# Optimization experiments

Hardware: AMD Instinct MI355X
Metric: run time of the kernel (lower is better)

Reference implementation:

```python
import jax, jax.numpy as jnp
import numpy as np

LAMBDA = 10.0      # sinkhorn_lambda from init_kwargs
N_ITERS = 100      # fixed Sinkhorn iteration count
B, T_MAX, D_MAX = 256, 256, 256
TP, DP = T_MAX + 1, D_MAX + 1   # expanded with births/deaths row+col
L = TP * DP                      # padded flat output length per example
EPS = 1e-12


def setup_inputs() -> dict:
    key = jax.random.key(0)
    k1, k2, k3 = jax.random.split(key, 3)
    affinity_scores = jax.random.uniform(k1, (B, T_MAX, D_MAX), dtype=jnp.float32)
    num_detections = jax.random.randint(k2, (B,), 32, D_MAX + 1, dtype=jnp.int32)
    num_tracklets = jax.random.randint(k3, (B,), 32, T_MAX + 1, dtype=jnp.int32)
    return {
        "affinity_scores": affinity_scores,
        "num_detections": num_detections,
        "num_tracklets": num_tracklets,
    }


def _sinkhorn_transport(aff, nd, nt):
    """Masked Sinkhorn on the expanded (nt+1)x(nd+1) matrix, padded to [TP,DP]."""
    r = jnp.arange(TP)
    c = jnp.arange(DP)
    row_valid = r <= nt          # nt tracklet rows + 1 births/deaths row
    col_valid = c <= nd
    interior = (r[:, None] < nt) & (c[None, :] < nd)
    aff_pad = jnp.pad(aff, ((0, 1), (0, 1)))
    aff_e = jnp.where(interior, aff_pad, 0.0)   # dummy row/col have affinity 0
    mask = (row_valid[:, None] & col_valid[None, :]).astype(aff.dtype)
    # cost = -affinity  =>  kernel K = exp(-lambda * cost) = exp(lambda * affinity)
    K = jnp.exp(LAMBDA * aff_e) * mask
    ndf = nd.astype(aff.dtype)
    ntf = nt.astype(aff.dtype)
    # target marginals: [1,...,1, length] on valid entries, 0 on padding
    row_sums = jnp.where(r < nt, 1.0, jnp.where(r == nt, ndf, 0.0))
    col_sums = jnp.where(c < nd, 1.0, jnp.where(c == nd, ntf, 0.0))
    u0 = jnp.zeros((TP,), aff.dtype)
    v0 = col_valid.astype(aff.dtype)

    def body(carry, _):
        u, v = carry
        u = jnp.where(row_valid, row_sums / (K @ v + EPS), 0.0)
        v = jnp.where(col_valid, col_sums / (K.T @ u + EPS), 0.0)
        return (u, v), None

    (u, v), _ = jax.lax.scan(body, (u0, v0), None, length=N_ITERS)
    transport = u[:, None] * K * v[None, :]
    return transport, interior, row_valid, col_valid


def _single(aff, nd, nt):
    transport, interior, row_valid, col_valid = _sinkhorn_transport(aff, nd, nt)
    r = jnp.arange(TP)
    c = jnp.arange(DP)

    # hard assignment on transport[:-1,:-1] (valid interior): mutual argmax
    neg_inf = jnp.array(-jnp.inf, transport.dtype)
    t_in = jnp.where(interior, transport, neg_inf)
    row_max = jnp.max(t_in, axis=1, keepdims=True)
    col_max = jnp.max(t_in, axis=0, keepdims=True)
    assign_in = interior & (t_in == row_max) & (t_in == col_max)
    # births/deaths: unmatched tracklets -> death col nd; unmatched detections -> birth row nt
    row_has = jnp.any(assign_in, axis=1)
    col_has = jnp.any(assign_in, axis=0)
    deaths = (r[:, None] < nt) & (c[None, :] == nd) & (~row_has)[:, None]
    births = (r[:, None] == nt) & (c[None, :] < nd) & (~col_has)[None, :]
    assignment = assign_in | deaths | births

    # flatten the (nt+1)x(nd+1) valid submatrix row-major, zero-pad to length L
    k = jnp.arange(L)
    length = (nt + 1) * (nd + 1)
    rr = jnp.clip(k // (nd + 1), 0, T_MAX)
    cc = k % (nd + 1)
    valid = k < length
    t_flat = jnp.where(valid, transport[rr, cc], 0.0)
    a_flat = jnp.where(valid, assignment[rr, cc], False)
    return t_flat, a_flat


def reference(affinity_scores, num_detections, num_tracklets):
    t_flat, a_flat = jax.vmap(_single)(affinity_scores, num_detections, num_tracklets)
    return t_flat, a_flat
```

## Files before the change

### kernel.cpp

```cpp
#include <hip/hip_runtime.h>


#define T_MAX   256
#define L_FLAT  (257 * 257)
#define N_ITERS 100
#define LAMBDA_F 10.0f
#define EPS_F    1e-12f

#define ROR1 0x121
#define ROR2 0x122
#define ROR4 0x124
#define ROR8 0x128

typedef short bf8   __attribute__((ext_vector_type(8)));
typedef float f32x4 __attribute__((ext_vector_type(4)));

struct F4 { float a, b, c, d; };

template<int CTRL>
__device__ __forceinline__ float dpp_addf(float x) {
    int t = __builtin_amdgcn_update_dpp(0, __float_as_int(x), CTRL, 0xF, 0xF, true);
    return x + __int_as_float(t);
}
__device__ __forceinline__ float swz16_addf(float x) {
    return x + __int_as_float(__builtin_amdgcn_ds_swizzle(__float_as_int(x), 0x401F));
}
__device__ __forceinline__ float swz16_maxf(float x) {
    return fmaxf(x, __int_as_float(__builtin_amdgcn_ds_swizzle(__float_as_int(x), 0x401F)));
}
__device__ __forceinline__ int swz16_ori(int x) {
    return x | __builtin_amdgcn_ds_swizzle(x, 0x401F);
}
__device__ __forceinline__ float fast_rcp(float x) {
#if __has_builtin(__builtin_amdgcn_rcpf)
    return __builtin_amdgcn_rcpf(x);
#else
    return 1.0f / x;
#endif
}
__device__ __forceinline__ unsigned short f2bf(float x) {
    unsigned u = __float_as_uint(x);
    return (unsigned short)((u + 0x7FFFu + ((u >> 16) & 1u)) >> 16);
}
__device__ __forceinline__ float bf2f(short s) {
    return __uint_as_float(((unsigned)(unsigned short)s) << 16);
}

__global__ __launch_bounds__(1024, 1) void assoc_sinkhorn_kernel(
    const float* __restrict__ aff,
    const int*   __restrict__ ndet,
    const int*   __restrict__ ntrk,
    float*       __restrict__ out_t,
    float*       __restrict__ out_a)
{
    const int b   = blockIdx.x;
    const int nd  = ndet[b];
    const int nt  = ntrk[b];
    const int tid = threadIdx.x;
    const int w   = tid >> 6;
    const int l   = tid & 63;
    const int lr  = l & 15;
    const int lk  = l >> 4;

    __shared__ __align__(16) unsigned short KTL[16 * 8 * 64 * 8];
    __shared__ __align__(16) unsigned short u_bf[256];
    __shared__ __align__(16) unsigned short v_bf[256];
    __shared__ __align__(16) float u_f[256];
    __shared__ __align__(16) float v_f[256];
    __shared__ __align__(16) float SuAcc[2];
    __shared__ __align__(16) float SvAcc[2];
    __shared__ __align__(16) float rm_s[256];
    __shared__ __align__(16) float cm_s[256];

    const float ndf = (float)nd;
    const float ntf = (float)nt;

    bf8 KA[8];
    const float* Ab = aff + (size_t)b * (T_MAX * T_MAX);

    const int myrow = 16 * w + lr;
    const int mycol = 16 * w + lr;
    unsigned short* myKTL = &KTL[(size_t)(w * 8 * 64 + l) * 8];

    {
        const bool rv = (myrow < nt);
        const float* rp = Ab + (size_t)myrow * T_MAX;
        #pragma unroll
        for (int t = 0; t < 8; ++t) {
            const int c0 = 32 * t + 8 * lk;
            const float4 x0 = *reinterpret_cast<const float4*>(rp + c0);
            const float4 x1 = *reinterpret_cast<const float4*>(rp + c0 + 4);
            const float e[8] = {x0.x, x0.y, x0.z, x0.w, x1.x, x1.y, x1.z, x1.w};
            bf8 kk;
            #pragma unroll
            for (int j = 0; j < 8; ++j) {
                const float val = (rv && (c0 + j) < nd) ? __expf(LAMBDA_F * e[j]) : 0.0f;
                kk[j] = (short)f2bf(val);
            }
            KA[t] = kk;
        }
    }
    {
        const bool cv = (mycol < nd);
        #pragma unroll
        for (int t = 0; t < 8; ++t) {
            const int r0 = 32 * t + 8 * lk;
            bf8 kk;
            #pragma unroll
            for (int j = 0; j < 8; ++j) {
                const float x = Ab[(size_t)(r0 + j) * T_MAX + mycol];
                const float val = (cv && (r0 + j) < nt) ? __expf(LAMBDA_F * x) : 0.0f;
                kk[j] = (short)f2bf(val);
            }
            *reinterpret_cast<bf8*>(myKTL + t * 512) = kk;
        }
    }

    if (tid < 256) v_bf[tid] = (tid < nd) ? f2bf(1.0f) : (unsigned short)0;
    if (tid == 0) {
        SuAcc[0] = 0.0f; SuAcc[1] = 0.0f;
        SvAcc[0] = ndf;  SvAcc[1] = 0.0f;
    }
    __syncthreads();

    float vbd = 1.0f;
    float ubd = 0.0f;

    const int r_a0 = 16 * w + 4 * lk;
    float u4[4] = {0.f, 0.f, 0.f, 0.f};
    float v0 = 0.0f;

    float rvm[4];
    #pragma unroll
    for (int q = 0; q < 4; ++q) rvm[q] = ((r_a0 + q) < nt) ? 1.0f : 0.0f;
    const float cvm = (mycol < nd) ? 1.0f : 0.0f;

    for (int it = 0; it < N_ITERS; ++it) {
        const int p = it & 1;
        const float Sv = SvAcc[p];

        f32x4 acc = {0.0f, 0.0f, 0.0f, 0.0f};
        #pragma unroll
        for (int t = 0; t < 8; ++t) {
            const bf8 VF = *reinterpret_cast<const bf8*>(&v_bf[32 * t + 8 * lk]);
            acc = __builtin_amdgcn_mfma_f32_16x16x32_bf16(KA[t], VF, acc, 0, 0, 0);
        }

        const float vbdE = vbd + EPS_F;
        #pragma unroll
        for (int q = 0; q < 4; ++q)
            u4[q] = rvm[q] * fast_rcp(acc[q] + vbdE);

        {
            float su = (u4[0] + u4[1]) + (u4[2] + u4[3]);
            su = swz16_addf(su);
            su += __shfl_xor(su, 32, 64);
            if (l == 0) atomicAdd(&SuAcc[p], su);
        }
        if (tid == 0) SuAcc[p ^ 1] = 0.0f;

        if (lr == 0) {
            const unsigned p01 = (unsigned)f2bf(u4[0]) | ((unsigned)f2bf(u4[1]) << 16);
            const unsigned p23 = (unsigned)f2bf(u4[2]) | ((unsigned)f2bf(u4[3]) << 16);
            *reinterpret_cast<uint2*>(&u_bf[r_a0]) = uint2{p01, p23};
        }
        __syncthreads();

        const float Su = SuAcc[p];
        const float ubd_new = ndf * fast_rcp(Sv + vbd + EPS_F);
        const float vbd_new = ntf * fast_rcp(Su + ubd_new + EPS_F);

        f32x4 qa = {0.0f, 0.0f, 0.0f, 0.0f};
        #pragma unroll
        for (int t = 0; t < 8; ++t) {
            const bf8 UF = *reinterpret_cast<const bf8*>(&u_bf[32 * t + 8 * lk]);
            const bf8 kb = *reinterpret_cast<const bf8*>(myKTL + t * 512);
            qa = __builtin_amdgcn_mfma_f32_16x16x32_bf16(UF, kb, qa, 0, 0, 0);
        }

        const float ubdE = ubd_new + EPS_F;
        v0 = cvm * fast_rcp(qa[0] + ubdE);

        {
            float sv = v0;
            sv = dpp_addf<ROR1>(sv);
            sv = dpp_addf<ROR2>(sv);
            sv = dpp_addf<ROR4>(sv);
            sv = dpp_addf<ROR8>(sv);
            if (l == 0) atomicAdd(&SvAcc[p ^ 1], sv);
        }
        if (tid == 0) SvAcc[p] = 0.0f;
        if (lk == 0) v_bf[mycol] = f2bf(v0);
        ubd = ubd_new;
        vbd = vbd_new;
        __syncthreads();
    }

    if (lr == 0) {
        f32x4 uf = {u4[0], u4[1], u4[2], u4[3]};
        *reinterpret_cast<f32x4*>(&u_f[r_a0]) = uf;
    }
    if (lk == 0) v_f[mycol] = v0;
    __syncthreads();

    float rm;
    {
        const float ur = u_f[myrow];
        float mm = 0.0f;
        #pragma unroll
        for (int t = 0; t < 8; ++t) {
            const f32x4 va = *reinterpret_cast<const f32x4*>(&v_f[32 * t + 8 * lk]);
            const f32x4 vb = *reinterpret_cast<const f32x4*>(&v_f[32 * t + 8 * lk + 4]);
            const float vj[8] = {va[0], va[1], va[2], va[3], vb[0], vb[1], vb[2], vb[3]};
            #pragma unroll
            for (int j = 0; j < 8; ++j) {
                const float tv = ur * bf2f(KA[t][j]) * vj[j];
                mm = fmaxf(mm, tv);
            }
        }
        mm = swz16_maxf(mm);
        mm = fmaxf(mm, __shfl_xor(mm, 32, 64));
        rm = mm;
        if (lk == 0) rm_s[myrow] = mm;
    }
    float cmv;
    {
        const float vc = v_f[mycol];
        float mm = 0.0f;
        #pragma unroll
        for (int t = 0; t < 8; ++t) {
            const int rb = 32 * t + 8 * lk;
            const bf8 kb = *reinterpret_cast<const bf8*>(myKTL + t * 512);
            const f32x4 ua = *reinterpret_cast<const f32x4*>(&u_f[rb]);
            const f32x4 ub = *reinterpret_cast<const f32x4*>(&u_f[rb + 4]);
            const float uj[8] = {ua[0], ua[1], ua[2], ua[3], ub[0], ub[1], ub[2], ub[3]};
            #pragma unroll
            for (int j = 0; j < 8; ++j) {
                const float tv = uj[j] * bf2f(kb[j]) * vc;
                mm = fmaxf(mm, tv);
            }
        }
        mm = swz16_maxf(mm);
        mm = fmaxf(mm, __shfl_xor(mm, 32, 64));
        cmv = mm;
        if (lk == 0) cm_s[mycol] = mm;
    }
    __syncthreads();

    float* Ot = out_t + (size_t)b * L_FLAT;
    float* Oa = out_a + (size_t)b * L_FLAT;
    const int stride = nd + 1;

    {
        const float vc = v_f[mycol];
        const bool cv = (mycol < nd);
        int has = 0;
        #pragma unroll
        for (int t = 0; t < 8; ++t) {
            const int rb = 32 * t + 8 * lk;
            const bf8 kb = *reinterpret_cast<const bf8*>(myKTL + t * 512);
            const f32x4 ua = *reinterpret_cast<const f32x4*>(&u_f[rb]);
            const f32x4 ub = *reinterpret_cast<const f32x4*>(&u_f[rb + 4]);
            const f32x4 ra = *reinterpret_cast<const f32x4*>(&rm_s[rb]);
            const f32x4 rb4 = *reinterpret_cast<const f32x4*>(&rm_s[rb + 4]);
            const float uj[8] = {ua[0], ua[1], ua[2], ua[3], ub[0], ub[1], ub[2], ub[3]};
            const float rj[8] = {ra[0], ra[1], ra[2], ra[3], rb4[0], rb4[1], rb4[2], rb4[3]};
            #pragma unroll
            for (int j = 0; j < 8; ++j) {
                const int rowj = rb + j;
                const float tv = uj[j] * bf2f(kb[j]) * vc;
                const bool bit = (rowj < nt) && cv && (tv == rj[j]) && (tv == cmv);
                has |= bit ? 1 : 0;
            }
        }
        has = swz16_ori(has);
        has |= __shfl_xor(has, 32, 64);
        if (lk == 0 && cv) {
            const int kk = nt * stride + mycol;
            Ot[kk] = ubd * vc;
            Oa[kk] = has ? 0.0f : 1.0f;
        }
    }
    if (tid == 0) {
        const int kk = nt * stride + nd;
        Ot[kk] = ubd * vbd;
        Oa[kk] = 0.0f;
    }

    {
        const float ur = u_f[myrow];
        const bool rv = (myrow < nt);
        int has = 0;
        #pragma unroll
        for (int t = 0; t < 8; ++t) {
            const int cb = 32 * t + 8 * lk;
            const f32x4 va  = *reinterpret_cast<const f32x4*>(&v_f[cb]);
            const f32x4 vb  = *reinterpret_cast<const f32x4*>(&v_f[cb + 4]);
            const f32x4 ca  = *reinterpret_cast<const f32x4*>(&cm_s[cb]);
            const f32x4 cb4 = *reinterpret_cast<const f32x4*>(&cm_s[cb + 4]);
            float tvs[8];
            float abs_[8];
            #pragma unroll
            for (int j = 0; j < 4; ++j) {
                const float tv = ur * bf2f(KA[t][j]) * va[j];
                const bool bit = rv && ((cb + j) < nd) && (tv == rm) && (tv == ca[j]);
                tvs[j] = tv; abs_[j] = bit ? 1.0f : 0.0f;
                has |= bit ? 1 : 0;
            }
            #pragma unroll
            for (int j = 0; j < 4; ++j) {
                const float tv = ur * bf2f(KA[t][4 + j]) * vb[j];
                const bool bit = rv && ((cb + 4 + j) < nd) && (tv == rm) && (tv == cb4[j]);
                tvs[4 + j] = tv; abs_[4 + j] = bit ? 1.0f : 0.0f;
                has |= bit ? 1 : 0;
            }
            if (rv) {
                float* OtR = Ot + (size_t)myrow * stride;
                float* OaR = Oa + (size_t)myrow * stride;
                #pragma unroll
                for (int g = 0; g < 2; ++g) {
                    const int c0 = cb + 4 * g;
                    if (c0 + 3 < nd) {
                        F4 ot = {tvs[4*g], tvs[4*g+1], tvs[4*g+2], tvs[4*g+3]};
                        F4 oa = {abs_[4*g], abs_[4*g+1], abs_[4*g+2], abs_[4*g+3]};
                        *reinterpret_cast<F4*>(OtR + c0) = ot;
                        *reinterpret_cast<F4*>(OaR + c0) = oa;
                    } else {
                        #pragma unroll
                        for (int j = 0; j < 4; ++j) {
                            if (c0 + j < nd) {
                                OtR[c0 + j] = tvs[4*g + j];
                                OaR[c0 + j] = abs_[4*g + j];
                            }
                        }
                    }
                }
            }
        }
        has = swz16_ori(has);
        has |= __shfl_xor(has, 32, 64);
        if (lk == 0 && rv) {
            const int kk = myrow * stride + nd;
            Ot[kk] = ur * vbd;
            Oa[kk] = has ? 0.0f : 1.0f;
        }
    }

    const int length = (nt + 1) * stride;
    for (int k = length + tid; k < L_FLAT; k += 1024) {
        Ot[k] = 0.0f;
        Oa[k] = 0.0f;
    }
}

extern "C" void kernel_launch(void* const* d_in, const int* in_sizes, int n_in,
                              void* d_out, int out_size, void* d_ws, size_t ws_size,
                              hipStream_t stream)
{
    const float* aff  = (const float*)d_in[0];
    const int*   ndet = (const int*)d_in[1];
    const int*   ntrk = (const int*)d_in[2];
    const int    Bn   = in_sizes[1];
    float* out_t = (float*)d_out;
    float* out_a = out_t + (size_t)Bn * L_FLAT;
    assoc_sinkhorn_kernel<<<dim3(Bn), dim3(1024), 0, stream>>>(aff, ndet, ntrk, out_t, out_a);
}
```

Baseline: 392.2 us.

## Replace MFMA K^T·u matvec with packed-bf16 scalar FMA dot products

The second Sinkhorn half-step (K^T u) no longer uses 16x16x32 MFMA, where only one output column of the 16 was useful. It now computes each column dot product with scalar FMAs over packed bf16 pairs. Each lane handles two columns over a 32-row slice, and the partial sums are reduced with DPP quad permutes and swizzles. The transposed K storage in shared memory is re-laid out as packed u32 pairs to match, and the post-loop column max and assignment checks are rewritten for the new layout. This removes the wasted MFMA work, but adds more VALU instructions and cross-lane reduction steps to every iteration.

```diff
diff --git a/kernel.cpp b/kernel.cpp
--- a/kernel.cpp
+++ b/kernel.cpp
@@ -7,13 +7,15 @@
 #define LAMBDA_F 10.0f
 #define EPS_F    1e-12f
 
-#define ROR1 0x121
-#define ROR2 0x122
-#define ROR4 0x124
-#define ROR8 0x128
+#define QX1   0xB1
+#define QX2   0x4E
+#define SWZ4  0x101F
+#define SWZ8  0x201F
+#define SWZ16 0x401F
 
 typedef short bf8   __attribute__((ext_vector_type(8)));
 typedef float f32x4 __attribute__((ext_vector_type(4)));
+typedef unsigned int u32x4 __attribute__((ext_vector_type(4)));
 
 struct F4 { float a, b, c, d; };
 
@@ -22,14 +24,27 @@
     int t = __builtin_amdgcn_update_dpp(0, __float_as_int(x), CTRL, 0xF, 0xF, true);
     return x + __int_as_float(t);
 }
-__device__ __forceinline__ float swz16_addf(float x) {
-    return x + __int_as_float(__builtin_amdgcn_ds_swizzle(__float_as_int(x), 0x401F));
-}
-__device__ __forceinline__ float swz16_maxf(float x) {
-    return fmaxf(x, __int_as_float(__builtin_amdgcn_ds_swizzle(__float_as_int(x), 0x401F)));
-}
-__device__ __forceinline__ int swz16_ori(int x) {
-    return x | __builtin_amdgcn_ds_swizzle(x, 0x401F);
+template<int CTRL>
+__device__ __forceinline__ float dpp_maxf(float x) {
+    int t = __builtin_amdgcn_update_dpp(0, __float_as_int(x), CTRL, 0xF, 0xF, true);
+    return fmaxf(x, __int_as_float(t));
+}
+template<int CTRL>
+__device__ __forceinline__ int dpp_ori(int x) {
+    int t = __builtin_amdgcn_update_dpp(0, x, CTRL, 0xF, 0xF, true);
+    return x | t;
+}
+template<int OFF>
+__device__ __forceinline__ float swz_addf(float x) {
+    return x + __int_as_float(__builtin_amdgcn_ds_swizzle(__float_as_int(x), OFF));
+}
+template<int OFF>
+__device__ __forceinline__ float swz_maxf(float x) {
+    return fmaxf(x, __int_as_float(__builtin_amdgcn_ds_swizzle(__float_as_int(x), OFF)));
+}
+template<int OFF>
+__device__ __forceinline__ int swz_ori(int x) {
+    return x | __builtin_amdgcn_ds_swizzle(x, OFF);
 }
 __device__ __forceinline__ float fast_rcp(float x) {
 #if __has_builtin(__builtin_amdgcn_rcpf)
@@ -44,6 +59,12 @@
 }
 __device__ __forceinline__ float bf2f(short s) {
     return __uint_as_float(((unsigned)(unsigned short)s) << 16);
+}
+__device__ __forceinline__ float bflo(unsigned u) {
+    return __uint_as_float(u << 16);
+}
+__device__ __forceinline__ float bfhi(unsigned u) {
+    return __uint_as_float(u & 0xFFFF0000u);
 }
 
 __global__ __launch_bounds__(1024, 1) void assoc_sinkhorn_kernel(
@@ -61,8 +82,10 @@
     const int l   = tid & 63;
     const int lr  = l & 15;
     const int lk  = l >> 4;
-
-    __shared__ __align__(16) unsigned short KTL[16 * 8 * 64 * 8];
+    const int cp  = l >> 3;
+    const int rc  = l & 7;
+
+    __shared__ __align__(16) unsigned KCL[16 * 8 * 64 * 4];
     __shared__ __align__(16) unsigned short u_bf[256];
     __shared__ __align__(16) unsigned short v_bf[256];
     __shared__ __align__(16) float u_f[256];
@@ -79,40 +102,48 @@
     const float* Ab = aff + (size_t)b * (T_MAX * T_MAX);
 
     const int myrow = 16 * w + lr;
-    const int mycol = 16 * w + lr;
-    unsigned short* myKTL = &KTL[(size_t)(w * 8 * 64 + l) * 8];
+    const int c0    = 16 * w + 2 * cp;
+    unsigned* myKC0 = &KCL[((w * 8 + 0) * 64 + l) * 4];
+    unsigned* myKC1 = &KCL[((w * 8 + 4) * 64 + l) * 4];
 
     {
         const bool rv = (myrow < nt);
         const float* rp = Ab + (size_t)myrow * T_MAX;
         #pragma unroll
         for (int t = 0; t < 8; ++t) {
-            const int c0 = 32 * t + 8 * lk;
-            const float4 x0 = *reinterpret_cast<const float4*>(rp + c0);
-            const float4 x1 = *reinterpret_cast<const float4*>(rp + c0 + 4);
+            const int cc0 = 32 * t + 8 * lk;
+            const float4 x0 = *reinterpret_cast<const float4*>(rp + cc0);
+            const float4 x1 = *reinterpret_cast<const float4*>(rp + cc0 + 4);
             const float e[8] = {x0.x, x0.y, x0.z, x0.w, x1.x, x1.y, x1.z, x1.w};
             bf8 kk;
             #pragma unroll
             for (int j = 0; j < 8; ++j) {
-                const float val = (rv && (c0 + j) < nd) ? __expf(LAMBDA_F * e[j]) : 0.0f;
+                const float val = (rv && (cc0 + j) < nd) ? __expf(LAMBDA_F * e[j]) : 0.0f;
                 kk[j] = (short)f2bf(val);
             }
             KA[t] = kk;
         }
     }
     {
-        const bool cv = (mycol < nd);
-        #pragma unroll
-        for (int t = 0; t < 8; ++t) {
-            const int r0 = 32 * t + 8 * lk;
-            bf8 kk;
-            #pragma unroll
-            for (int j = 0; j < 8; ++j) {
-                const float x = Ab[(size_t)(r0 + j) * T_MAX + mycol];
-                const float val = (cv && (r0 + j) < nt) ? __expf(LAMBDA_F * x) : 0.0f;
-                kk[j] = (short)f2bf(val);
-            }
-            *reinterpret_cast<bf8*>(myKTL + t * 512) = kk;
+        #pragma unroll
+        for (int j = 0; j < 2; ++j) {
+            const int col = c0 + j;
+            const bool cv = (col < nd);
+            unsigned* dst = (j == 0) ? myKC0 : myKC1;
+            #pragma unroll
+            for (int g = 0; g < 4; ++g) {
+                u32x4 pk;
+                #pragma unroll
+                for (int s = 0; s < 4; ++s) {
+                    const int r = 32 * rc + 8 * g + 2 * s;
+                    const float x0 = Ab[(size_t)r * T_MAX + col];
+                    const float x1 = Ab[(size_t)(r + 1) * T_MAX + col];
+                    const float f0 = (cv && r     < nt) ? __expf(LAMBDA_F * x0) : 0.0f;
+                    const float f1 = (cv && r + 1 < nt) ? __expf(LAMBDA_F * x1) : 0.0f;
+                    pk[s] = (unsigned)f2bf(f0) | ((unsigned)f2bf(f1) << 16);
+                }
+                *reinterpret_cast<u32x4*>(dst + g * 256) = pk;
+            }
         }
     }
 
@@ -128,12 +159,13 @@
 
     const int r_a0 = 16 * w + 4 * lk;
     float u4[4] = {0.f, 0.f, 0.f, 0.f};
-    float v0 = 0.0f;
+    float v0 = 0.0f, v1 = 0.0f;
 
     float rvm[4];
     #pragma unroll
     for (int q = 0; q < 4; ++q) rvm[q] = ((r_a0 + q) < nt) ? 1.0f : 0.0f;
-    const float cvm = (mycol < nd) ? 1.0f : 0.0f;
+    const float cvm0 = (c0     < nd) ? 1.0f : 0.0f;
+    const float cvm1 = (c0 + 1 < nd) ? 1.0f : 0.0f;
 
     for (int it = 0; it < N_ITERS; ++it) {
         const int p = it & 1;
@@ -153,7 +185,7 @@
 
         {
             float su = (u4[0] + u4[1]) + (u4[2] + u4[3]);
-            su = swz16_addf(su);
+            su = swz_addf<SWZ16>(su);
             su += __shfl_xor(su, 32, 64);
             if (l == 0) atomicAdd(&SuAcc[p], su);
         }
@@ -170,27 +202,43 @@
         const float ubd_new = ndf * fast_rcp(Sv + vbd + EPS_F);
         const float vbd_new = ntf * fast_rcp(Su + ubd_new + EPS_F);
 
-        f32x4 qa = {0.0f, 0.0f, 0.0f, 0.0f};
-        #pragma unroll
-        for (int t = 0; t < 8; ++t) {
-            const bf8 UF = *reinterpret_cast<const bf8*>(&u_bf[32 * t + 8 * lk]);
-            const bf8 kb = *reinterpret_cast<const bf8*>(myKTL + t * 512);
-            qa = __builtin_amdgcn_mfma_f32_16x16x32_bf16(UF, kb, qa, 0, 0, 0);
-        }
-
         const float ubdE = ubd_new + EPS_F;
-        v0 = cvm * fast_rcp(qa[0] + ubdE);
-
+        float t0 = 0.0f, t1 = 0.0f;
         {
-            float sv = v0;
-            sv = dpp_addf<ROR1>(sv);
-            sv = dpp_addf<ROR2>(sv);
-            sv = dpp_addf<ROR4>(sv);
-            sv = dpp_addf<ROR8>(sv);
+            const u32x4* ub = reinterpret_cast<const u32x4*>(&u_bf[32 * rc]);
+            #pragma unroll
+            for (int g = 0; g < 4; ++g) {
+                const u32x4 U  = ub[g];
+                const u32x4 K0 = *reinterpret_cast<const u32x4*>(myKC0 + g * 256);
+                const u32x4 K1 = *reinterpret_cast<const u32x4*>(myKC1 + g * 256);
+                #pragma unroll
+                for (int s = 0; s < 4; ++s) {
+                    const float ulo = bflo(U[s]);
+                    const float uhi = bfhi(U[s]);
+                    t0 = fmaf(bflo(K0[s]), ulo, t0);
+                    t0 = fmaf(bfhi(K0[s]), uhi, t0);
+                    t1 = fmaf(bflo(K1[s]), ulo, t1);
+                    t1 = fmaf(bfhi(K1[s]), uhi, t1);
+                }
+            }
+        }
+        t0 = dpp_addf<QX1>(t0); t0 = dpp_addf<QX2>(t0); t0 = swz_addf<SWZ4>(t0);
+        t1 = dpp_addf<QX1>(t1); t1 = dpp_addf<QX2>(t1); t1 = swz_addf<SWZ4>(t1);
+
+        v0 = cvm0 * fast_rcp(t0 + ubdE);
+        v1 = cvm1 * fast_rcp(t1 + ubdE);
+
+        {
+            float sv = v0 + v1;
+            sv = swz_addf<SWZ8>(sv);
+            sv = swz_addf<SWZ16>(sv);
+            sv += __shfl_xor(sv, 32, 64);
             if (l == 0) atomicAdd(&SvAcc[p ^ 1], sv);
         }
         if (tid == 0) SvAcc[p] = 0.0f;
-        if (lk == 0) v_bf[mycol] = f2bf(v0);
+        if (rc == 0)
+            *reinterpret_cast<unsigned*>(&v_bf[c0]) =
+                (unsigned)f2bf(v0) | ((unsigned)f2bf(v1) << 16);
         ubd = ubd_new;
         vbd = vbd_new;
         __syncthreads();
@@ -200,7 +248,10 @@
         f32x4 uf = {u4[0], u4[1], u4[2], u4[3]};
         *reinterpret_cast<f32x4*>(&u_f[r_a0]) = uf;
     }
-    if (lk == 0) v_f[mycol] = v0;
+    if (rc == 0) {
+        v_f[c0]     = v0;
+        v_f[c0 + 1] = v1;
+    }
     __syncthreads();
 
     float rm;
@@ -218,32 +269,36 @@
                 mm = fmaxf(mm, tv);
             }
         }
-        mm = swz16_maxf(mm);
+        mm = swz_maxf<SWZ16>(mm);
         mm = fmaxf(mm, __shfl_xor(mm, 32, 64));
         rm = mm;
         if (lk == 0) rm_s[myrow] = mm;
     }
-    float cmv;
-    {
-        const float vc = v_f[mycol];
-        float mm = 0.0f;
-        #pragma unroll
-        for (int t = 0; t < 8; ++t) {
-            const int rb = 32 * t + 8 * lk;
-            const bf8 kb = *reinterpret_cast<const bf8*>(myKTL + t * 512);
-            const f32x4 ua = *reinterpret_cast<const f32x4*>(&u_f[rb]);
-            const f32x4 ub = *reinterpret_cast<const f32x4*>(&u_f[rb + 4]);
-            const float uj[8] = {ua[0], ua[1], ua[2], ua[3], ub[0], ub[1], ub[2], ub[3]};
-            #pragma unroll
-            for (int j = 0; j < 8; ++j) {
-                const float tv = uj[j] * bf2f(kb[j]) * vc;
-                mm = fmaxf(mm, tv);
-            }
-        }
-        mm = swz16_maxf(mm);
-        mm = fmaxf(mm, __shfl_xor(mm, 32, 64));
-        cmv = mm;
-        if (lk == 0) cm_s[mycol] = mm;
+    float cmv0 = 0.0f, cmv1 = 0.0f;
+    {
+        const float vc0 = v_f[c0];
+        const float vc1 = v_f[c0 + 1];
+        #pragma unroll
+        for (int g = 0; g < 4; ++g) {
+            const u32x4 K0 = *reinterpret_cast<const u32x4*>(myKC0 + g * 256);
+            const u32x4 K1 = *reinterpret_cast<const u32x4*>(myKC1 + g * 256);
+            const f32x4 ua  = *reinterpret_cast<const f32x4*>(&u_f[32 * rc + 8 * g]);
+            const f32x4 ub2 = *reinterpret_cast<const f32x4*>(&u_f[32 * rc + 8 * g + 4]);
+            const float uu[8] = {ua[0], ua[1], ua[2], ua[3], ub2[0], ub2[1], ub2[2], ub2[3]};
+            #pragma unroll
+            for (int s = 0; s < 4; ++s) {
+                cmv0 = fmaxf(cmv0, fmaxf((uu[2*s] * bflo(K0[s])) * vc0,
+                                         (uu[2*s+1] * bfhi(K0[s])) * vc0));
+                cmv1 = fmaxf(cmv1, fmaxf((uu[2*s] * bflo(K1[s])) * vc1,
+                                         (uu[2*s+1] * bfhi(K1[s])) * vc1));
+            }
+        }
+        cmv0 = dpp_maxf<QX1>(cmv0); cmv0 = dpp_maxf<QX2>(cmv0); cmv0 = swz_maxf<SWZ4>(cmv0);
+        cmv1 = dpp_maxf<QX1>(cmv1); cmv1 = dpp_maxf<QX2>(cmv1); cmv1 = swz_maxf<SWZ4>(cmv1);
+        if (rc == 0) {
+            cm_s[c0]     = cmv0;
+            cm_s[c0 + 1] = cmv1;
+        }
     }
     __syncthreads();
 
@@ -252,33 +307,45 @@
     const int stride = nd + 1;
 
     {
-        const float vc = v_f[mycol];
-        const bool cv = (mycol < nd);
-        int has = 0;
-        #pragma unroll
-        for (int t = 0; t < 8; ++t) {
-            const int rb = 32 * t + 8 * lk;
-            const bf8 kb = *reinterpret_cast<const bf8*>(myKTL + t * 512);
-            const f32x4 ua = *reinterpret_cast<const f32x4*>(&u_f[rb]);
-            const f32x4 ub = *reinterpret_cast<const f32x4*>(&u_f[rb + 4]);
-            const f32x4 ra = *reinterpret_cast<const f32x4*>(&rm_s[rb]);
-            const f32x4 rb4 = *reinterpret_cast<const f32x4*>(&rm_s[rb + 4]);
-            const float uj[8] = {ua[0], ua[1], ua[2], ua[3], ub[0], ub[1], ub[2], ub[3]};
-            const float rj[8] = {ra[0], ra[1], ra[2], ra[3], rb4[0], rb4[1], rb4[2], rb4[3]};
-            #pragma unroll
-            for (int j = 0; j < 8; ++j) {
-                const int rowj = rb + j;
-                const float tv = uj[j] * bf2f(kb[j]) * vc;
-                const bool bit = (rowj < nt) && cv && (tv == rj[j]) && (tv == cmv);
-                has |= bit ? 1 : 0;
-            }
-        }
-        has = swz16_ori(has);
-        has |= __shfl_xor(has, 32, 64);
-        if (lk == 0 && cv) {
-            const int kk = nt * stride + mycol;
-            Ot[kk] = ubd * vc;
-            Oa[kk] = has ? 0.0f : 1.0f;
+        const float vc[2]  = {v_f[c0], v_f[c0 + 1]};
+        const float cmx[2] = {cmv0, cmv1};
+        int has0 = 0, has1 = 0;
+        #pragma unroll
+        for (int g = 0; g < 4; ++g) {
+            const u32x4 K0 = *reinterpret_cast<const u32x4*>(myKC0 + g * 256);
+            const u32x4 K1 = *reinterpret_cast<const u32x4*>(myKC1 + g * 256);
+            const f32x4 ua  = *reinterpret_cast<const f32x4*>(&u_f[32 * rc + 8 * g]);
+            const f32x4 ub2 = *reinterpret_cast<const f32x4*>(&u_f[32 * rc + 8 * g + 4]);
+            const f32x4 ra  = *reinterpret_cast<const f32x4*>(&rm_s[32 * rc + 8 * g]);
+            const f32x4 rb2 = *reinterpret_cast<const f32x4*>(&rm_s[32 * rc + 8 * g + 4]);
+            const float uu[8] = {ua[0], ua[1], ua[2], ua[3], ub2[0], ub2[1], ub2[2], ub2[3]};
+            const float rr[8] = {ra[0], ra[1], ra[2], ra[3], rb2[0], rb2[1], rb2[2], rb2[3]};
+            #pragma unroll
+            for (int s = 0; s < 4; ++s) {
+                const int r = 32 * rc + 8 * g + 2 * s;
+                const float t00 = (uu[2*s]   * bflo(K0[s])) * vc[0];
+                const float t01 = (uu[2*s+1] * bfhi(K0[s])) * vc[0];
+                const float t10 = (uu[2*s]   * bflo(K1[s])) * vc[1];
+                const float t11 = (uu[2*s+1] * bfhi(K1[s])) * vc[1];
+                if ((r     < nt) && (c0     < nd) && t00 == rr[2*s]   && t00 == cmx[0]) has0 = 1;
+                if ((r + 1 < nt) && (c0     < nd) && t01 == rr[2*s+1] && t01 == cmx[0]) has0 = 1;
+                if ((r     < nt) && (c0 + 1 < nd) && t10 == rr[2*s]   && t10 == cmx[1]) has1 = 1;
+                if ((r + 1 < nt) && (c0 + 1 < nd) && t11 == rr[2*s+1] && t11 == cmx[1]) has1 = 1;
+            }
+        }
+        has0 = dpp_ori<QX1>(has0); has0 = dpp_ori<QX2>(has0); has0 = swz_ori<SWZ4>(has0);
+        has1 = dpp_ori<QX1>(has1); has1 = dpp_ori<QX2>(has1); has1 = swz_ori<SWZ4>(has1);
+        if (rc == 0) {
+            if (c0 < nd) {
+                const int kk = nt * stride + c0;
+                Ot[kk] = ubd * vc[0];
+                Oa[kk] = has0 ? 0.0f : 1.0f;
+            }
+            if (c0 + 1 < nd) {
+                const int kk = nt * stride + c0 + 1;
+                Ot[kk] = ubd * vc[1];
+                Oa[kk] = has1 ? 0.0f : 1.0f;
+            }
         }
     }
     if (tid == 0) {
@@ -319,25 +386,25 @@
                 float* OaR = Oa + (size_t)myrow * stride;
                 #pragma unroll
                 for (int g = 0; g < 2; ++g) {
-                    const int c0 = cb + 4 * g;
-                    if (c0 + 3 < nd) {
+                    const int cc0 = cb + 4 * g;
+                    if (cc0 + 3 < nd) {
                         F4 ot = {tvs[4*g], tvs[4*g+1], tvs[4*g+2], tvs[4*g+3]};
                         F4 oa = {abs_[4*g], abs_[4*g+1], abs_[4*g+2], abs_[4*g+3]};
-                        *reinterpret_cast<F4*>(OtR + c0) = ot;
-                        *reinterpret_cast<F4*>(OaR + c0) = oa;
+                        *reinterpret_cast<F4*>(OtR + cc0) = ot;
+                        *reinterpret_cast<F4*>(OaR + cc0) = oa;
                     } else {
                         #pragma unroll
                         for (int j = 0; j < 4; ++j) {
-                            if (c0 + j < nd) {
-                                OtR[c0 + j] = tvs[4*g + j];
-                                OaR[c0 + j] = abs_[4*g + j];
+                            if (cc0 + j < nd) {
+                                OtR[cc0 + j] = tvs[4*g + j];
+                                OaR[cc0 + j] = abs_[4*g + j];
                             }
                         }
                     }
                 }
             }
         }
-        has = swz16_ori(has);
+        has = swz_ori<SWZ16>(has);
         has |= __shfl_xor(has, 32, 64);
         if (lk == 0 && rv) {
             const int kk = myrow * stride + nd;
```

Measured after the change: 503.3 us. 1.28x slower.

## Keep both K tiles in AGPRs and feed MFMA via inline asm

Applied to the files above, without the earlier changes.

The transposed K tile moves out of LDS and into a second register array. Inline-asm MFMA wrappers take their operands from accumulator registers, so the Sinkhorn loop no longer issues LDS loads for K^T. To free those registers, the epilogue recomputes K from global affinities with exp and bf16 rounding instead of reusing the register tiles. The manual s_nop padding adds fixed stalls around each MFMA chain, and the epilogue now does extra global reads and exp work.

```diff
diff --git a/kernel.cpp b/kernel.cpp
--- a/kernel.cpp
+++ b/kernel.cpp
@@ -16,6 +16,17 @@
 typedef float f32x4 __attribute__((ext_vector_type(4)));
 
 struct F4 { float a, b, c, d; };
+
+__device__ __forceinline__ void mfma_AV(f32x4& d, const bf8& a, const bf8& b) {
+    asm volatile("v_mfma_f32_16x16x32_bf16 %0, %1, %2, %0"
+                 : "+v"(d) : "a"(a), "v"(b));
+}
+__device__ __forceinline__ void mfma_VA(f32x4& d, const bf8& a, const bf8& b) {
+    asm volatile("v_mfma_f32_16x16x32_bf16 %0, %1, %2, %0"
+                 : "+v"(d) : "v"(a), "a"(b));
+}
+__device__ __forceinline__ void mfma_pre()  { asm volatile("s_nop 1"); }
+__device__ __forceinline__ void mfma_post() { asm volatile("s_nop 7\n\ts_nop 7"); }
 
 template<int CTRL>
 __device__ __forceinline__ float dpp_addf(float x) {
@@ -62,7 +73,6 @@
     const int lr  = l & 15;
     const int lk  = l >> 4;
 
-    __shared__ __align__(16) unsigned short KTL[16 * 8 * 64 * 8];
     __shared__ __align__(16) unsigned short u_bf[256];
     __shared__ __align__(16) unsigned short v_bf[256];
     __shared__ __align__(16) float u_f[256];
@@ -75,12 +85,12 @@
     const float ndf = (float)nd;
     const float ntf = (float)nt;
 
-    bf8 KA[8];
+    bf8 KA_A[8];
+    bf8 KB_A[8];
     const float* Ab = aff + (size_t)b * (T_MAX * T_MAX);
 
     const int myrow = 16 * w + lr;
     const int mycol = 16 * w + lr;
-    unsigned short* myKTL = &KTL[(size_t)(w * 8 * 64 + l) * 8];
 
     {
         const bool rv = (myrow < nt);
@@ -97,7 +107,7 @@
                 const float val = (rv && (c0 + j) < nd) ? __expf(LAMBDA_F * e[j]) : 0.0f;
                 kk[j] = (short)f2bf(val);
             }
-            KA[t] = kk;
+            KA_A[t] = kk;
         }
     }
     {
@@ -112,7 +122,7 @@
                 const float val = (cv && (r0 + j) < nt) ? __expf(LAMBDA_F * x) : 0.0f;
                 kk[j] = (short)f2bf(val);
             }
-            *reinterpret_cast<bf8*>(myKTL + t * 512) = kk;
+            KB_A[t] = kk;
         }
     }
 
@@ -140,11 +150,13 @@
         const float Sv = SvAcc[p];
 
         f32x4 acc = {0.0f, 0.0f, 0.0f, 0.0f};
+        mfma_pre();
         #pragma unroll
         for (int t = 0; t < 8; ++t) {
             const bf8 VF = *reinterpret_cast<const bf8*>(&v_bf[32 * t + 8 * lk]);
-            acc = __builtin_amdgcn_mfma_f32_16x16x32_bf16(KA[t], VF, acc, 0, 0, 0);
-        }
+            mfma_AV(acc, KA_A[t], VF);
+        }
+        mfma_post();
 
         const float vbdE = vbd + EPS_F;
         #pragma unroll
@@ -171,12 +183,13 @@
         const float vbd_new = ntf * fast_rcp(Su + ubd_new + EPS_F);
 
         f32x4 qa = {0.0f, 0.0f, 0.0f, 0.0f};
+        mfma_pre();
         #pragma unroll
         for (int t = 0; t < 8; ++t) {
             const bf8 UF = *reinterpret_cast<const bf8*>(&u_bf[32 * t + 8 * lk]);
-            const bf8 kb = *reinterpret_cast<const bf8*>(myKTL + t * 512);
-            qa = __builtin_amdgcn_mfma_f32_16x16x32_bf16(UF, kb, qa, 0, 0, 0);
-        }
+            mfma_VA(qa, UF, KB_A[t]);
+        }
+        mfma_post();
 
         const float ubdE = ubd_new + EPS_F;
         v0 = cvm * fast_rcp(qa[0] + ubdE);
@@ -203,18 +216,27 @@
     if (lk == 0) v_f[mycol] = v0;
     __syncthreads();
 
+    const bool rv_e = (myrow < nt);
+    const bool cv_e = (mycol < nd);
+
     float rm;
     {
         const float ur = u_f[myrow];
+        const float* rp = Ab + (size_t)myrow * T_MAX;
         float mm = 0.0f;
         #pragma unroll
         for (int t = 0; t < 8; ++t) {
-            const f32x4 va = *reinterpret_cast<const f32x4*>(&v_f[32 * t + 8 * lk]);
-            const f32x4 vb = *reinterpret_cast<const f32x4*>(&v_f[32 * t + 8 * lk + 4]);
+            const int c0 = 32 * t + 8 * lk;
+            const float4 x0 = *reinterpret_cast<const float4*>(rp + c0);
+            const float4 x1 = *reinterpret_cast<const float4*>(rp + c0 + 4);
+            const float e[8] = {x0.x, x0.y, x0.z, x0.w, x1.x, x1.y, x1.z, x1.w};
+            const f32x4 va = *reinterpret_cast<const f32x4*>(&v_f[c0]);
+            const f32x4 vb = *reinterpret_cast<const f32x4*>(&v_f[c0 + 4]);
             const float vj[8] = {va[0], va[1], va[2], va[3], vb[0], vb[1], vb[2], vb[3]};
             #pragma unroll
             for (int j = 0; j < 8; ++j) {
-                const float tv = ur * bf2f(KA[t][j]) * vj[j];
+                const float kv = (rv_e && (c0 + j) < nd) ? __expf(LAMBDA_F * e[j]) : 0.0f;
+                const float tv = ur * bf2f((short)f2bf(kv)) * vj[j];
                 mm = fmaxf(mm, tv);
             }
         }
@@ -230,13 +252,14 @@
         #pragma unroll
         for (int t = 0; t < 8; ++t) {
             const int rb = 32 * t + 8 * lk;
-            const bf8 kb = *reinterpret_cast<const bf8*>(myKTL + t * 512);
             const f32x4 ua = *reinterpret_cast<const f32x4*>(&u_f[rb]);
             const f32x4 ub = *reinterpret_cast<const f32x4*>(&u_f[rb + 4]);
             const float uj[8] = {ua[0], ua[1], ua[2], ua[3], ub[0], ub[1], ub[2], ub[3]};
             #pragma unroll
             for (int j = 0; j < 8; ++j) {
-                const float tv = uj[j] * bf2f(kb[j]) * vc;
+                const float x = Ab[(size_t)(rb + j) * T_MAX + mycol];
+                const float kv = (cv_e && (rb + j) < nt) ? __expf(LAMBDA_F * x) : 0.0f;
+                const float tv = uj[j] * bf2f((short)f2bf(kv)) * vc;
                 mm = fmaxf(mm, tv);
             }
         }
@@ -253,12 +276,10 @@
 
     {
         const float vc = v_f[mycol];
-        const bool cv = (mycol < nd);
         int has = 0;
         #pragma unroll
         for (int t = 0; t < 8; ++t) {
             const int rb = 32 * t + 8 * lk;
-            const bf8 kb = *reinterpret_cast<const bf8*>(myKTL + t * 512);
             const f32x4 ua = *reinterpret_cast<const f32x4*>(&u_f[rb]);
             const f32x4 ub = *reinterpret_cast<const f32x4*>(&u_f[rb + 4]);
             const f32x4 ra = *reinterpret_cast<const f32x4*>(&rm_s[rb]);
@@ -268,14 +289,16 @@
             #pragma unroll
             for (int j = 0; j < 8; ++j) {
                 const int rowj = rb + j;
-                const float tv = uj[j] * bf2f(kb[j]) * vc;
-                const bool bit = (rowj < nt) && cv && (tv == rj[j]) && (tv == cmv);
+                const float x = Ab[(size_t)rowj * T_MAX + mycol];
+                const float kv = (cv_e && rowj < nt) ? __expf(LAMBDA_F * x) : 0.0f;
+                const float tv = uj[j] * bf2f((short)f2bf(kv)) * vc;
+                const bool bit = (rowj < nt) && cv_e && (tv == rj[j]) && (tv == cmv);
                 has |= bit ? 1 : 0;
             }
         }
         has = swz16_ori(has);
         has |= __shfl_xor(has, 32, 64);
-        if (lk == 0 && cv) {
+        if (lk == 0 && cv_e) {
             const int kk = nt * stride + mycol;
             Ot[kk] = ubd * vc;
             Oa[kk] = has ? 0.0f : 1.0f;
@@ -289,32 +312,31 @@
 
     {
         const float ur = u_f[myrow];
-        const bool rv = (myrow < nt);
+        const float* rp = Ab + (size_t)myrow * T_MAX;
         int has = 0;
         #pragma unroll
         for (int t = 0; t < 8; ++t) {
             const int cb = 32 * t + 8 * lk;
+            const float4 x0 = *reinterpret_cast<const float4*>(rp + cb);
+            const float4 x1 = *reinterpret_cast<const float4*>(rp + cb + 4);
+            const float e[8] = {x0.x, x0.y, x0.z, x0.w, x1.x, x1.y, x1.z, x1.w};
             const f32x4 va  = *reinterpret_cast<const f32x4*>(&v_f[cb]);
             const f32x4 vb  = *reinterpret_cast<const f32x4*>(&v_f[cb + 4]);
             const f32x4 ca  = *reinterpret_cast<const f32x4*>(&cm_s[cb]);
             const f32x4 cb4 = *reinterpret_cast<const f32x4*>(&cm_s[cb + 4]);
+            const float vj[8] = {va[0], va[1], va[2], va[3], vb[0], vb[1], vb[2], vb[3]};
+            const float cj[8] = {ca[0], ca[1], ca[2], ca[3], cb4[0], cb4[1], cb4[2], cb4[3]};
             float tvs[8];
             float abs_[8];
             #pragma unroll
-            for (int j = 0; j < 4; ++j) {
-                const float tv = ur * bf2f(KA[t][j]) * va[j];
-                const bool bit = rv && ((cb + j) < nd) && (tv == rm) && (tv == ca[j]);
+            for (int j = 0; j < 8; ++j) {
+                const float kv = (rv_e && (cb + j) < nd) ? __expf(LAMBDA_F * e[j]) : 0.0f;
+                const float tv = ur * bf2f((short)f2bf(kv)) * vj[j];
+                const bool bit = rv_e && ((cb + j) < nd) && (tv == rm) && (tv == cj[j]);
                 tvs[j] = tv; abs_[j] = bit ? 1.0f : 0.0f;
                 has |= bit ? 1 : 0;
             }
-            #pragma unroll
-            for (int j = 0; j < 4; ++j) {
-                const float tv = ur * bf2f(KA[t][4 + j]) * vb[j];
-                const bool bit = rv && ((cb + 4 + j) < nd) && (tv == rm) && (tv == cb4[j]);
-                tvs[4 + j] = tv; abs_[4 + j] = bit ? 1.0f : 0.0f;
-                has |= bit ? 1 : 0;
-            }
-            if (rv) {
+            if (rv_e) {
                 float* OtR = Ot + (size_t)myrow * stride;
                 float* OaR = Oa + (size_t)myrow * stride;
                 #pragma unroll
@@ -339,7 +361,7 @@
         }
         has = swz16_ori(has);
         has |= __shfl_xor(has, 32, 64);
-        if (lk == 0 && rv) {
+        if (lk == 0 && rv_e) {
             const int kk = myrow * stride + nd;
             Ot[kk] = ur * vbd;
             Oa[kk] = has ? 0.0f : 1.0f;
```

Result: slower. 668.1 us (+70.4%).
